# Optimization experiments

Measured on AMD Instinct MI355X. Metric: run time of the kernel, lower is better.

## Reference

```python
import jax, jax.numpy as jnp
import numpy as np

N, E, H, G = 50000, 500000, 64, 64


def _ln(x, g, b):
    m = jnp.mean(x, -1, keepdims=True)
    v = jnp.var(x, -1, keepdims=True)
    return (x - m) * jax.lax.rsqrt(v + 1e-5) * g + b


def _mlp_ln(x, w1, b1, w2, b2, g, be):
    # Linear -> ReLU -> (Dropout eval no-op) -> Linear -> LayerNorm
    h = jax.nn.relu(x @ w1 + b1)
    return _ln(h @ w2 + b2, g, be)


def setup_inputs() -> dict:
    key = jax.random.key(0)
    ks = jax.random.split(key, 24)
    w = lambda i, s: jax.random.normal(ks[i], s, dtype=jnp.float32) * 0.1
    z = lambda s: jnp.zeros(s, jnp.float32)
    o = lambda s: jnp.ones(s, jnp.float32)
    inp = {
        'x': jax.random.normal(ks[0], (N, 3), dtype=jnp.float32),
        'edge_index': jax.random.randint(ks[1], (2, E), 0, N),
        'edge_attr': jax.random.normal(ks[2], (E, 3), dtype=jnp.float32),
        'batch': jnp.sort(jax.random.randint(ks[3], (N,), 0, G)),
        'ne_w1': w(4, (3, H)), 'ne_b1': z((H,)), 'ne_w2': w(5, (H, H)), 'ne_b2': z((H,)), 'ne_g': o((H,)), 'ne_be': z((H,)),
        'ee_w1': w(6, (3, H)), 'ee_b1': z((H,)), 'ee_w2': w(7, (H, H)), 'ee_b2': z((H,)), 'ee_g': o((H,)), 'ee_be': z((H,)),
        'gin0_eps': z((1,)), 'gin0_w1': w(8, (H, H)), 'gin0_b1': z((H,)), 'gin0_w2': w(9, (H, H)), 'gin0_b2': z((H,)), 'gin0_g': o((H,)), 'gin0_be': z((H,)),
        'gin1_eps': z((1,)), 'gin1_w1': w(10, (H, H)), 'gin1_b1': z((H,)), 'gin1_w2': w(11, (H, H)), 'gin1_b2': z((H,)), 'gin1_g': o((H,)), 'gin1_be': z((H,)),
        'gp_w': w(12, (H, H)), 'gp_b': z((H,)), 'gp_g': o((H,)), 'gp_be': z((H,)),
        'ep_w1': w(13, (4 * H, 2 * H)), 'ep_b1': z((2 * H,)),
        'ep_w2': w(14, (2 * H, H)), 'ep_b2': z((H,)),
        'ep_w3': w(15, (H, 1)), 'ep_b3': z((1,)),
    }
    return inp


def reference(x, edge_index, edge_attr, batch,
              ne_w1, ne_b1, ne_w2, ne_b2, ne_g, ne_be,
              ee_w1, ee_b1, ee_w2, ee_b2, ee_g, ee_be,
              gin0_eps, gin0_w1, gin0_b1, gin0_w2, gin0_b2, gin0_g, gin0_be,
              gin1_eps, gin1_w1, gin1_b1, gin1_w2, gin1_b2, gin1_g, gin1_be,
              gp_w, gp_b, gp_g, gp_be,
              ep_w1, ep_b1, ep_w2, ep_b2, ep_w3, ep_b3):
    src, dst = edge_index[0], edge_index[1]
    # encoders
    h = _mlp_ln(x, ne_w1, ne_b1, ne_w2, ne_b2, ne_g, ne_be)            # [N, H]
    ef = _mlp_ln(edge_attr, ee_w1, ee_b1, ee_w2, ee_b2, ee_g, ee_be)   # [E, H]
    # GINEConv layer 0: mlp((1+eps)*x + scatter_add(relu(x_src + e)))
    msg = jax.nn.relu(h[src] + ef)
    aggr = jnp.zeros_like(h).at[dst].add(msg)
    h = _mlp_ln((1.0 + gin0_eps) * h + aggr, gin0_w1, gin0_b1, gin0_w2, gin0_b2, gin0_g, gin0_be)
    h = jax.nn.relu(h)  # inter-layer activation (dropout eval no-op)
    # GINEConv layer 1
    msg = jax.nn.relu(h[src] + ef)
    aggr = jnp.zeros_like(h).at[dst].add(msg)
    h = _mlp_ln((1.0 + gin1_eps) * h + aggr, gin1_w1, gin1_b1, gin1_w2, gin1_b2, gin1_g, gin1_be)
    # global mean pool over graphs
    seg = jax.ops.segment_sum(h, batch, num_segments=G)                            # [G, H]
    cnt = jax.ops.segment_sum(jnp.ones((h.shape[0], 1), h.dtype), batch, num_segments=G)
    gp = seg / jnp.maximum(cnt, 1.0)
    gf = _ln(jax.nn.relu(gp @ gp_w + gp_b), gp_g, gp_be)                           # [G, H]
    # edge predictor on [src | dst | global | edge] = [E, 4H]
    c = jnp.concatenate([h[src], h[dst], gf[batch[src]], ef], axis=-1)
    t = jnp.tanh(c @ ep_w1 + ep_b1)
    t = jnp.tanh(t @ ep_w2 + ep_b2)
    return jax.nn.sigmoid(t @ ep_w3 + ep_b3)  # [E, 1]
```

## Files before the change

### kernel.cpp

```cpp
#include <hip/hip_runtime.h>
#include <hip/hip_bf16.h>

typedef unsigned int uint;
typedef unsigned short ushort;
typedef __attribute__((ext_vector_type(8))) short short8;
typedef __attribute__((ext_vector_type(4))) float floatx4;

__device__ __forceinline__ float bf2f(ushort u) { return __uint_as_float(((uint)u) << 16); }
__device__ __forceinline__ ushort f2bf(float f) {
  uint u = __float_as_uint(f);
  u += 0x7fffu + ((u >> 16) & 1u);
  return (ushort)(u >> 16);
}
__device__ __forceinline__ uint pk2(float a, float b) {
  return (uint)f2bf(a) | ((uint)f2bf(b) << 16);
}
__device__ __forceinline__ float ldf(const void* p, long i, int m) {
  if (m) return bf2f(((const ushort*)p)[i]);
  return ((const float*)p)[i];
}
__device__ __forceinline__ int get_md(const uint* mdp) {
  return (mdp[0] == 0x3F800000u) ? 0 : 1;
}
__device__ __forceinline__ float fast_rcp(float x) { return __builtin_amdgcn_rcpf(x); }
__device__ __forceinline__ float tanh_fast(float x) {
  float e = __builtin_amdgcn_exp2f(2.8853900818f * x);
  return fmaf(-2.f, fast_rcp(1.f + e), 1.f);
}
__device__ __forceinline__ float sigmoid_fast(float x) {
  float e = __builtin_amdgcn_exp2f(-1.4426950409f * x);
  return fast_rcp(1.f + e);
}

__global__ __launch_bounds__(256) void k_enc_mfma(
    const void* __restrict__ in, int R,
    const void* __restrict__ w1, const void* __restrict__ b1,
    const ushort* __restrict__ w2sw_, const void* __restrict__ b2,
    const void* __restrict__ gam, const void* __restrict__ bet,
    ushort* __restrict__ outp, const uint* __restrict__ mdp)
{
  __shared__ float xs[64*3];
  __shared__ float w1s[192], b1s[64], b2s[64], gs[64], bs2[64];
  __shared__ __align__(16) ushort T_s[64 * 72];
  int md = get_md(mdp);
  int tid = threadIdx.x;
  long e0 = (long)blockIdx.x * 64;
  if (tid < 192) {
    w1s[tid] = ldf(w1, tid, md);
    int row = tid / 3, cc = tid - row*3;
    long e = e0 + row;
    xs[tid] = (e < R) ? ldf(in, e*3 + cc, md) : 0.f;
  }
  if (tid < 64) { b1s[tid] = ldf(b1, tid, md); b2s[tid] = ldf(b2, tid, md);
                  gs[tid] = ldf(gam, tid, md); bs2[tid] = ldf(bet, tid, md); }
  __syncthreads();
  int lane = tid & 63, wv = tid >> 6;
  int quad = lane >> 4, mm = lane & 15;
  float x0 = xs[(wv*16 + mm)*3 + 0];
  float x1 = xs[(wv*16 + mm)*3 + 1];
  float x2 = xs[(wv*16 + mm)*3 + 2];
  short8 af[2];
#pragma unroll
  for (int s = 0; s < 2; ++s) {
#pragma unroll
    for (int j = 0; j < 8; ++j) {
      int f = s*32 + quad*8 + j;
      float hv = fmaxf(b1s[f] + x0*w1s[f] + x1*w1s[64+f] + x2*w1s[128+f], 0.f);
      af[s][j] = (short)f2bf(hv);
    }
  }
  floatx4 acc[4] = {};
  const short8* Bp = (const short8*)w2sw_;
#pragma unroll
  for (int s = 0; s < 2; ++s) {
#pragma unroll
    for (int t = 0; t < 4; ++t) {
      short8 b = Bp[(s*4 + t)*64 + lane];
      acc[t] = __builtin_amdgcn_mfma_f32_16x16x32_bf16(af[s], b, acc[t], 0, 0, 0);
    }
  }
  float vv[4][4];
#pragma unroll
  for (int t = 0; t < 4; ++t) {
    float bb = b2s[mm + 16*t];
#pragma unroll
    for (int r = 0; r < 4; ++r) vv[t][r] = acc[t][r] + bb;
  }
  float mr[4], vr[4];
#pragma unroll
  for (int r = 0; r < 4; ++r) {
    float s = vv[0][r] + vv[1][r] + vv[2][r] + vv[3][r];
#pragma unroll
    for (int off = 1; off < 16; off <<= 1) s += __shfl_xor(s, off);
    mr[r] = s * 0.015625f;
    float q = 0.f;
#pragma unroll
    for (int t = 0; t < 4; ++t) { float d = vv[t][r] - mr[r]; q = fmaf(d, d, q); }
#pragma unroll
    for (int off = 1; off < 16; off <<= 1) q += __shfl_xor(q, off);
    vr[r] = rsqrtf(q * 0.015625f + 1e-5f);
  }
#pragma unroll
  for (int t = 0; t < 4; ++t) {
    int col = mm + 16*t;
    float g = gs[col], be = bs2[col];
#pragma unroll
    for (int r = 0; r < 4; ++r)
      T_s[(wv*16 + quad*4 + r)*72 + col] = f2bf((vv[t][r] - mr[r]) * vr[r] * g + be);
  }
  __syncthreads();
#pragma unroll
  for (int i = 0; i < 2; ++i) {
    int gi = tid + 256*i;
    int row = gi >> 3, c = gi & 7;
    long e = e0 + row;
    if (e < R)
      ((uint4*)(outp + e*64))[c] = *(const uint4*)&T_s[row*72 + c*8];
  }
}

__global__ __launch_bounds__(256) void k_deg(
    const int* __restrict__ ei, int* __restrict__ deg, int E_)
{
  int e = blockIdx.x * 256 + threadIdx.x;
  if (e < E_) atomicAdd(&deg[ei[E_ + e]], 1);
}

__global__ __launch_bounds__(256) void k_scan1(
    const int* __restrict__ deg, int* __restrict__ rs, int* __restrict__ bsum, int Nn)
{
  __shared__ int ls[256];
  int tid = threadIdx.x;
  int i = blockIdx.x * 256 + tid;
  int v = (i < Nn) ? deg[i] : 0;
  ls[tid] = v;
  __syncthreads();
  for (int off = 1; off < 256; off <<= 1) {
    int t = (tid >= off) ? ls[tid - off] : 0;
    __syncthreads();
    ls[tid] += t;
    __syncthreads();
  }
  if (i < Nn) rs[i] = ls[tid] - v;
  if (tid == 255) bsum[blockIdx.x] = ls[255];
}

__global__ __launch_bounds__(256) void k_scan2(
    int* __restrict__ bsum, int nb, int* __restrict__ rs, int Nn)
{
  __shared__ int ls[256];
  int tid = threadIdx.x;
  int chunk = (nb + 255) / 256;
  int c0 = tid * chunk, c1 = min(c0 + chunk, nb);
  int sum = 0;
  for (int i = c0; i < c1; ++i) sum += bsum[i];
  ls[tid] = sum;
  __syncthreads();
  for (int off = 1; off < 256; off <<= 1) {
    int t = (tid >= off) ? ls[tid - off] : 0;
    __syncthreads();
    ls[tid] += t;
    __syncthreads();
  }
  int run = ls[tid] - sum;
  for (int i = c0; i < c1; ++i) { int d = bsum[i]; bsum[i] = run; run += d; }
  if (tid == 255) rs[Nn] = ls[255];
}

__global__ __launch_bounds__(256) void k_scan3(
    int* __restrict__ rs, int* __restrict__ cur,
    const int* __restrict__ bsum, int Nn)
{
  int i = blockIdx.x * 256 + threadIdx.x;
  if (i < Nn) {
    int v = rs[i] + bsum[blockIdx.x];
    rs[i] = v;
    cur[i] = v;
  }
}

__global__ __launch_bounds__(256) void k_fill(
    const int* __restrict__ ei, int* __restrict__ cur, int* __restrict__ eidx, int E_)
{
  int e = blockIdx.x * 256 + threadIdx.x;
  if (e < E_) {
    int d = ei[E_ + e];
    int p = atomicAdd(&cur[d], 1);
    eidx[p] = e;
  }
}

__global__ __launch_bounds__(256) void k_aggr(
    const ushort* __restrict__ hbu, const ushort* __restrict__ efu,
    const int* __restrict__ ei, const int* __restrict__ rs,
    const int* __restrict__ eidx, float* __restrict__ aggr, int Nn, int E_)
{
  int gw = (blockIdx.x * 256 + threadIdx.x) >> 6;
  int j = threadIdx.x & 63;
  if (gw >= Nn) return;
  int s0 = rs[gw], s1 = rs[gw + 1];
  float acc = 0.f;
  int idx = s0;
  for (; idx + 2 <= s1; idx += 2) {
    int e1 = eidx[idx], e2 = eidx[idx + 1];
    int sA = ei[e1], sB = ei[e2];
    float hA = bf2f(hbu[(long)sA*64 + j]);
    float fA = bf2f(efu[(long)e1*64 + j]);
    float hB = bf2f(hbu[(long)sB*64 + j]);
    float fB = bf2f(efu[(long)e2*64 + j]);
    acc += fmaxf(hA + fA, 0.f) + fmaxf(hB + fB, 0.f);
  }
  if (idx < s1) {
    int e1 = eidx[idx];
    int sA = ei[e1];
    acc += fmaxf(bf2f(hbu[(long)sA*64 + j]) + bf2f(efu[(long)e1*64 + j]), 0.f);
  }
  aggr[(long)gw*64 + j] = acc;
}

__global__ __launch_bounds__(256) void k_gine_mfma(
    const ushort* __restrict__ hbin, const float* __restrict__ aggr, int Nn,
    const void* __restrict__ epsp,
    const ushort* __restrict__ w1sw_, const void* __restrict__ b1,
    const ushort* __restrict__ w2sw_, const void* __restrict__ b2,
    const void* __restrict__ gam, const void* __restrict__ bet,
    ushort* __restrict__ hbout, int post_relu, const uint* __restrict__ mdp)
{
  __shared__ __align__(16) ushort Ws1[4096], Ws2[4096];
  __shared__ __align__(16) ushort T_s[64 * 72];
  __shared__ float b1s[64], b2s[64], gs[64], bs2[64];
  int md = get_md(mdp);
  int tid = threadIdx.x;
  {
    const uint4* p1 = (const uint4*)w1sw_;
    const uint4* p2 = (const uint4*)w2sw_;
    ((uint4*)Ws1)[tid] = p1[tid];
    ((uint4*)Ws1)[tid + 256] = p1[tid + 256];
    ((uint4*)Ws2)[tid] = p2[tid];
    ((uint4*)Ws2)[tid + 256] = p2[tid + 256];
  }
  if (tid < 64) { b1s[tid] = ldf(b1, tid, md); b2s[tid] = ldf(b2, tid, md);
                  gs[tid] = ldf(gam, tid, md); bs2[tid] = ldf(bet, tid, md); }
  float ope = 1.f + ldf(epsp, 0, md);
  int lane = tid & 63, wv = tid >> 6;
  int quad = lane >> 4, mm = lane & 15;
  long node = (long)blockIdx.x * 64 + wv*16 + mm;
  long nc = (node < Nn) ? node : (long)(Nn - 1);
  const ushort* hrow = hbin + nc*64;
  const float*  arow = aggr + nc*64;
  short8 af[2];
#pragma unroll
  for (int s = 0; s < 2; ++s) {
    int c = s*4 + quad;
    short8 hv = *(const short8*)(hrow + c*8);
    float4 a0 = *(const float4*)(arow + c*8);
    float4 a1 = *(const float4*)(arow + c*8 + 4);
    float uu[8];
    uu[0] = fmaf(bf2f((ushort)hv[0]), ope, a0.x);
    uu[1] = fmaf(bf2f((ushort)hv[1]), ope, a0.y);
    uu[2] = fmaf(bf2f((ushort)hv[2]), ope, a0.z);
    uu[3] = fmaf(bf2f((ushort)hv[3]), ope, a0.w);
    uu[4] = fmaf(bf2f((ushort)hv[4]), ope, a1.x);
    uu[5] = fmaf(bf2f((ushort)hv[5]), ope, a1.y);
    uu[6] = fmaf(bf2f((ushort)hv[6]), ope, a1.z);
    uu[7] = fmaf(bf2f((ushort)hv[7]), ope, a1.w);
#pragma unroll
    for (int j = 0; j < 8; ++j) af[s][j] = (short)f2bf(uu[j]);
  }
  __syncthreads();
  floatx4 acc[4] = {};
#pragma unroll
  for (int s = 0; s < 2; ++s) {
#pragma unroll
    for (int t = 0; t < 4; ++t) {
      short8 b = *(const short8*)&Ws1[((s*4 + t)*64 + lane)*8];
      acc[t] = __builtin_amdgcn_mfma_f32_16x16x32_bf16(af[s], b, acc[t], 0, 0, 0);
    }
  }
#pragma unroll
  for (int t = 0; t < 4; ++t) {
    int col = mm + 16*t;
    float bb = b1s[col];
#pragma unroll
    for (int r = 0; r < 4; ++r)
      T_s[(wv*16 + quad*4 + r)*72 + col] = f2bf(fmaxf(acc[t][r] + bb, 0.f));
  }
  __syncthreads();
  short8 af2[2];
#pragma unroll
  for (int s = 0; s < 2; ++s)
    af2[s] = *(const short8*)&T_s[(wv*16 + mm)*72 + s*32 + quad*8];
  floatx4 acc2[4] = {};
#pragma unroll
  for (int s = 0; s < 2; ++s) {
#pragma unroll
    for (int t = 0; t < 4; ++t) {
      short8 b = *(const short8*)&Ws2[((s*4 + t)*64 + lane)*8];
      acc2[t] = __builtin_amdgcn_mfma_f32_16x16x32_bf16(af2[s], b, acc2[t], 0, 0, 0);
    }
  }
  float vv[4][4];
#pragma unroll
  for (int t = 0; t < 4; ++t) {
    float bb = b2s[mm + 16*t];
#pragma unroll
    for (int r = 0; r < 4; ++r) vv[t][r] = acc2[t][r] + bb;
  }
  float mr[4], vr[4];
#pragma unroll
  for (int r = 0; r < 4; ++r) {
    float s = vv[0][r] + vv[1][r] + vv[2][r] + vv[3][r];
#pragma unroll
    for (int off = 1; off < 16; off <<= 1) s += __shfl_xor(s, off);
    mr[r] = s * 0.015625f;
    float q = 0.f;
#pragma unroll
    for (int t = 0; t < 4; ++t) { float d = vv[t][r] - mr[r]; q = fmaf(d, d, q); }
#pragma unroll
    for (int off = 1; off < 16; off <<= 1) q += __shfl_xor(q, off);
    vr[r] = rsqrtf(q * 0.015625f + 1e-5f);
  }
  __syncthreads();
#pragma unroll
  for (int t = 0; t < 4; ++t) {
    int col = mm + 16*t;
    float g = gs[col], be = bs2[col];
#pragma unroll
    for (int r = 0; r < 4; ++r) {
      float o = (vv[t][r] - mr[r]) * vr[r] * g + be;
      if (post_relu) o = fmaxf(o, 0.f);
      T_s[(wv*16 + quad*4 + r)*72 + col] = f2bf(o);
    }
  }
  __syncthreads();
#pragma unroll
  for (int i = 0; i < 2; ++i) {
    int gi = tid + 256*i;
    int row = gi >> 3, c = gi & 7;
    long n2 = (long)blockIdx.x * 64 + row;
    if (n2 < Nn)
      ((uint4*)(hbout + n2*64))[c] = *(const uint4*)&T_s[row*72 + c*8];
  }
}

__global__ __launch_bounds__(256) void k_pool_f(
    const ushort* __restrict__ hbu, const int* __restrict__ batch,
    float* __restrict__ gsum, float* __restrict__ gcnt, int Nn)
{
  int gw = (blockIdx.x * 256 + threadIdx.x) >> 6;
  int j = threadIdx.x & 63;
  long r0 = (long)gw * 64;
  if (r0 >= Nn) return;
  long rend = min(r0 + 64, (long)Nn);
  float acc = 0.f; int cur = batch[r0]; int run = 0;
  for (long r = r0; r < rend; ++r) {
    int g = batch[r];
    if (g != cur) {
      atomicAdd(&gsum[cur*64 + j], acc);
      if (j == 0) atomicAdd(&gcnt[cur], (float)run);
      acc = 0.f; run = 0; cur = g;
    }
    acc += bf2f(hbu[r*64 + j]);
    run++;
  }
  atomicAdd(&gsum[cur*64 + j], acc);
  if (j == 0) atomicAdd(&gcnt[cur], (float)run);
}

__global__ __launch_bounds__(64) void k_pool_fin_f(
    const float* __restrict__ gsum, const float* __restrict__ gcnt,
    const void* __restrict__ gpw, const void* __restrict__ gpb,
    const void* __restrict__ gpg, const void* __restrict__ gpbe,
    ushort* __restrict__ gfb, const uint* __restrict__ mdp)
{
  __shared__ float wgs[4096];
  __shared__ float us[64];
  int md = get_md(mdp);
  int j = threadIdx.x;
  int g = blockIdx.x;
  for (int i = j; i < 4096; i += 64) wgs[i] = ldf(gpw, i, md);
  float ic = 1.f / fmaxf(gcnt[g], 1.f);
  us[j] = gsum[g*64 + j] * ic;
  __syncthreads();
  float t = ldf(gpb, j, md);
#pragma unroll
  for (int k = 0; k < 64; ++k) t = fmaf(us[k], wgs[k*64 + j], t);
  t = fmaxf(t, 0.f);
  float m = t;
#pragma unroll
  for (int off = 1; off < 64; off <<= 1) m += __shfl_xor(m, off);
  m *= 0.015625f;
  float d = t - m;
  float v = d * d;
#pragma unroll
  for (int off = 1; off < 64; off <<= 1) v += __shfl_xor(v, off);
  float rs = rsqrtf(v * 0.015625f + 1e-5f);
  gfb[g*64 + j] = f2bf(d * rs * ldf(gpg, j, md) + ldf(gpbe, j, md));
}

__global__ __launch_bounds__(256) void k_swz(
    const void* __restrict__ w1, const void* __restrict__ w2,
    const void* __restrict__ w2e, const void* __restrict__ w2n,
    const void* __restrict__ gw10, const void* __restrict__ gw20,
    const void* __restrict__ gw11, const void* __restrict__ gw21,
    ushort* __restrict__ w1sw, ushort* __restrict__ w2sw,
    ushort* __restrict__ ew2sw, ushort* __restrict__ nw2sw,
    ushort* __restrict__ g0w1sw, ushort* __restrict__ g0w2sw,
    ushort* __restrict__ g1w1sw, ushort* __restrict__ g1w2sw,
    const uint* __restrict__ mdp)
{
  int md = get_md(mdp);
  int i = blockIdx.x * 256 + threadIdx.x;
  if (i < 32768) {
    int q = i & 7, lane = (i >> 3) & 63, tt = (i >> 9) & 7, s = i >> 12;
    int k = s*32 + (lane >> 4)*8 + q, n = (lane & 15) + 16*tt;
    w1sw[i] = f2bf(ldf(w1, k*128 + n, md));
  }
  if (i < 8192) {
    int q = i & 7, lane = (i >> 3) & 63, tt = (i >> 9) & 3, s = i >> 11;
    int k = s*32 + (lane >> 4)*8 + q, n = (lane & 15) + 16*tt;
    int src = k*64 + n;
    w2sw[i]   = f2bf(ldf(w2,   src, md));
    ew2sw[i]  = f2bf(ldf(w2e,  src, md));
    nw2sw[i]  = f2bf(ldf(w2n,  src, md));
    g0w1sw[i] = f2bf(ldf(gw10, src, md));
    g0w2sw[i] = f2bf(ldf(gw20, src, md));
    g1w1sw[i] = f2bf(ldf(gw11, src, md));
    g1w2sw[i] = f2bf(ldf(gw21, src, md));
  }
}

__global__ __launch_bounds__(256) void k_pred_mfma(
    const ushort* __restrict__ hb, const ushort* __restrict__ efu,
    const ushort* __restrict__ gfb, const int* __restrict__ ei,
    const int* __restrict__ batch,
    const ushort* __restrict__ w1sw, const ushort* __restrict__ w2sw,
    const void* __restrict__ pb1, const void* __restrict__ pb2,
    const void* __restrict__ pw3, const void* __restrict__ pb3,
    void* __restrict__ out, int E_, const uint* __restrict__ mdp)
{
  __shared__ __align__(16) ushort Ws[8192];
  __shared__ __align__(16) ushort T_s[64 * 136];
  __shared__ float b1s[128], b2s[64], w3s[64];
  int md = get_md(mdp);
  int tid = threadIdx.x;
  if (tid < 128) b1s[tid] = ldf(pb1, tid, md);
  if (tid < 64) { b2s[tid] = ldf(pb2, tid, md); w3s[tid] = ldf(pw3, tid, md); }
  long e0 = (long)blockIdx.x * 64;
  int lane = tid & 63, wv = tid >> 6;
  int quad = lane >> 4, mm = lane & 15;
  long e = e0 + wv*16 + mm;
  if (e >= E_) e = E_ - 1;
  int si = ei[e];
  int di = ei[E_ + e];
  int gi = batch[si];
  const short8* hsrc = (const short8*)(hb  + (long)si*64);
  const short8* hdst = (const short8*)(hb  + (long)di*64);
  const short8* gsrc = (const short8*)(gfb + (long)gi*64);
  const short8* esrc = (const short8*)(efu + e*64);
  short8 af[8];
  af[0] = hsrc[quad]; af[1] = hsrc[4 + quad];
  af[2] = hdst[quad]; af[3] = hdst[4 + quad];
  af[4] = gsrc[quad]; af[5] = gsrc[4 + quad];
  af[6] = esrc[quad]; af[7] = esrc[4 + quad];
  floatx4 acc[8] = {};
  for (int q = 0; q < 4; ++q) {
    __syncthreads();
    const uint4* wp = (const uint4*)(w1sw + q*8192);
#pragma unroll
    for (int i = 0; i < 4; ++i)
      ((uint4*)Ws)[tid + 256*i] = wp[tid + 256*i];
    __syncthreads();
#pragma unroll
    for (int s4 = 0; s4 < 2; ++s4) {
      short8 a = af[q*2 + s4];
#pragma unroll
      for (int t = 0; t < 8; ++t) {
        short8 b = *(const short8*)&Ws[((s4*8 + t)*64 + lane)*8];
        acc[t] = __builtin_amdgcn_mfma_f32_16x16x32_bf16(a, b, acc[t], 0, 0, 0);
      }
    }
  }
#pragma unroll
  for (int t = 0; t < 8; ++t) {
    float bb = b1s[mm + 16*t];
#pragma unroll
    for (int r = 0; r < 4; ++r)
      T_s[(16*wv + quad*4 + r)*136 + mm + 16*t] = f2bf(tanh_fast(acc[t][r] + bb));
  }
  __syncthreads();
  {
    const uint4* wp2 = (const uint4*)w2sw;
#pragma unroll
    for (int i = 0; i < 4; ++i)
      ((uint4*)Ws)[tid + 256*i] = wp2[tid + 256*i];
  }
  __syncthreads();
  floatx4 acc2[4] = {};
#pragma unroll
  for (int s2 = 0; s2 < 4; ++s2) {
    short8 a = *(const short8*)&T_s[(16*wv + mm)*136 + s2*32 + quad*8];
#pragma unroll
    for (int t = 0; t < 4; ++t) {
      short8 b = *(const short8*)&Ws[((s2*4 + t)*64 + lane)*8];
      acc2[t] = __builtin_amdgcn_mfma_f32_16x16x32_bf16(a, b, acc2[t], 0, 0, 0);
    }
  }
  float p0 = 0.f, p1 = 0.f, p2 = 0.f, p3 = 0.f;
#pragma unroll
  for (int t = 0; t < 4; ++t) {
    int col = mm + 16*t;
    float bb = b2s[col], w3v = w3s[col];
    p0 = fmaf(tanh_fast(acc2[t][0] + bb), w3v, p0);
    p1 = fmaf(tanh_fast(acc2[t][1] + bb), w3v, p1);
    p2 = fmaf(tanh_fast(acc2[t][2] + bb), w3v, p2);
    p3 = fmaf(tanh_fast(acc2[t][3] + bb), w3v, p3);
  }
#pragma unroll
  for (int off = 1; off < 16; off <<= 1) {
    p0 += __shfl_xor(p0, off);
    p1 += __shfl_xor(p1, off);
    p2 += __shfl_xor(p2, off);
    p3 += __shfl_xor(p3, off);
  }
  if (mm == 0) {
    float b3 = ldf(pb3, 0, md);
    long eb = e0 + 16*wv + quad*4;
    float ps[4] = {p0, p1, p2, p3};
#pragma unroll
    for (int r = 0; r < 4; ++r) {
      if (eb + r < E_) {
        float sg = sigmoid_fast(ps[r] + b3);
        if (md) ((ushort*)out)[eb + r] = f2bf(sg);
        else    ((float*)out)[eb + r]  = sg;
      }
    }
  }
}

extern "C" void kernel_launch(void* const* d_in, const int* in_sizes, int n_in,
                              void* d_out, int out_size, void* d_ws, size_t ws_size,
                              hipStream_t stream)
{
  const void* x     = d_in[0];
  const int*  ei    = (const int*)d_in[1];
  const void* eattr = d_in[2];
  const int*  batch = (const int*)d_in[3];
  const void* ne_w1 = d_in[4];  const void* ne_b1 = d_in[5];
  const void* ne_w2 = d_in[6];  const void* ne_b2 = d_in[7];
  const void* ne_g  = d_in[8];  const void* ne_be = d_in[9];
  const void* ee_w1 = d_in[10]; const void* ee_b1 = d_in[11];
  const void* ee_w2 = d_in[12]; const void* ee_b2 = d_in[13];
  const void* ee_g  = d_in[14]; const void* ee_be = d_in[15];
  const void* g0_ep = d_in[16];
  const void* g0_w1 = d_in[17]; const void* g0_b1 = d_in[18];
  const void* g0_w2 = d_in[19]; const void* g0_b2 = d_in[20];
  const void* g0_g  = d_in[21]; const void* g0_be = d_in[22];
  const void* g1_ep = d_in[23];
  const void* g1_w1 = d_in[24]; const void* g1_b1 = d_in[25];
  const void* g1_w2 = d_in[26]; const void* g1_b2 = d_in[27];
  const void* g1_g  = d_in[28]; const void* g1_be = d_in[29];
  const void* gp_w  = d_in[30]; const void* gp_b  = d_in[31];
  const void* gp_g  = d_in[32]; const void* gp_be = d_in[33];
  const void* ep_w1 = d_in[34]; const void* ep_b1 = d_in[35];
  const void* ep_w2 = d_in[36]; const void* ep_b2 = d_in[37];
  const void* ep_w3 = d_in[38]; const void* ep_b3 = d_in[39];

  int N = in_sizes[3];
  int E = in_sizes[1] / 2;
  const uint* mdp = (const uint*)ne_g;

  char* ws = (char*)d_ws;
  size_t off = 0;
  auto alloc = [&](size_t bytes) { char* p = ws + off; off += (bytes + 255) & ~(size_t)255; return p; };
  ushort* hb     = (ushort*)alloc((size_t)N * 64 * 2);
  ushort* efu    = (ushort*)alloc((size_t)E * 64 * 2);
  float*  aggr   = (float*) alloc((size_t)N * 64 * 4);
  float*  gsum   = (float*) alloc(64 * 64 * 4);
  float*  gcnt   = (float*) alloc(64 * 4);
  ushort* gfb    = (ushort*)alloc(64 * 64 * 2);
  ushort* w1sw   = (ushort*)alloc(32768 * 2);
  ushort* w2sw   = (ushort*)alloc(8192 * 2);
  ushort* ew2sw  = (ushort*)alloc(8192 * 2);
  ushort* nw2sw  = (ushort*)alloc(8192 * 2);
  ushort* g0w1sw = (ushort*)alloc(8192 * 2);
  ushort* g0w2sw = (ushort*)alloc(8192 * 2);
  ushort* g1w1sw = (ushort*)alloc(8192 * 2);
  ushort* g1w2sw = (ushort*)alloc(8192 * 2);
  int*    deg    = (int*)   alloc((size_t)N * 4);
  int*    rs     = (int*)   alloc((size_t)(N + 1) * 4);
  int*    cur    = (int*)   alloc((size_t)N * 4);
  int*    eidx   = (int*)   alloc((size_t)E * 4);
  int*    bsum   = (int*)   alloc((size_t)((N + 255) / 256) * 4);
  (void)ws_size; (void)n_in; (void)out_size;

  int gN = (N + 255) / 256;
  int gE = (E + 255) / 256;
  int gE64 = (E + 63) / 64;
  int gN64 = (N + 63) / 64;
  int gAggr = (int)(((long)N * 64 + 255) / 256);
  int gPool = ((N + 63) / 64 + 3) / 4;

  hipMemsetAsync(deg, 0, (size_t)N * 4, stream);
  hipMemsetAsync(gsum, 0, 64 * 64 * 4 + 256, stream);

  k_swz<<<128, 256, 0, stream>>>(ep_w1, ep_w2, ee_w2, ne_w2, g0_w1, g0_w2, g1_w1, g1_w2,
                                 w1sw, w2sw, ew2sw, nw2sw,
                                 g0w1sw, g0w2sw, g1w1sw, g1w2sw, mdp);
  k_deg<<<gE, 256, 0, stream>>>(ei, deg, E);
  k_scan1<<<gN, 256, 0, stream>>>(deg, rs, bsum, N);
  k_scan2<<<1, 256, 0, stream>>>(bsum, gN, rs, N);
  k_scan3<<<gN, 256, 0, stream>>>(rs, cur, bsum, N);
  k_fill<<<gE, 256, 0, stream>>>(ei, cur, eidx, E);
  k_enc_mfma<<<gN64, 256, 0, stream>>>(x, N, ne_w1, ne_b1, nw2sw, ne_b2, ne_g, ne_be, hb, mdp);
  k_enc_mfma<<<gE64, 256, 0, stream>>>(eattr, E, ee_w1, ee_b1, ew2sw, ee_b2, ee_g, ee_be, efu, mdp);
  k_aggr<<<gAggr, 256, 0, stream>>>(hb, efu, ei, rs, eidx, aggr, N, E);
  k_gine_mfma<<<gN64, 256, 0, stream>>>(hb, aggr, N, g0_ep, g0w1sw, g0_b1, g0w2sw, g0_b2,
                                        g0_g, g0_be, hb, 1, mdp);
  k_aggr<<<gAggr, 256, 0, stream>>>(hb, efu, ei, rs, eidx, aggr, N, E);
  k_gine_mfma<<<gN64, 256, 0, stream>>>(hb, aggr, N, g1_ep, g1w1sw, g1_b1, g1w2sw, g1_b2,
                                        g1_g, g1_be, hb, 0, mdp);
  k_pool_f<<<gPool, 256, 0, stream>>>(hb, batch, gsum, gcnt, N);
  k_pool_fin_f<<<64, 64, 0, stream>>>(gsum, gcnt, gp_w, gp_b, gp_g, gp_be, gfb, mdp);
  k_pred_mfma<<<gE64, 256, 0, stream>>>(hb, efu, gfb, ei, batch, w1sw, w2sw,
                                        ep_b1, ep_b2, ep_w3, ep_b3, d_out, E, mdp);
}
```

Measured before the change: 475.6 us.

## Store (edge,src) pairs in CSR and process 128 edges per predictor block

The CSR fill now stores the source node next to each edge id as an int2, so the aggregation kernel skips a dependent gather through edge_index. The edge predictor block now handles two 64-edge tiles at once, so each staged weight chunk in shared memory feeds twice as many MFMAs and the per-block weight reloads are halved. In exchange the predictor uses more registers and shared memory per block, which may lower occupancy, and the CSR array doubles in size.

```diff
diff --git a/kernel.cpp b/kernel.cpp
--- a/kernel.cpp
+++ b/kernel.cpp
@@ -180,20 +180,22 @@
 }
 
 __global__ __launch_bounds__(256) void k_fill(
-    const int* __restrict__ ei, int* __restrict__ cur, int* __restrict__ eidx, int E_)
+    const int* __restrict__ ei, int* __restrict__ cur,
+    int2* __restrict__ ep, int E_)
 {
   int e = blockIdx.x * 256 + threadIdx.x;
   if (e < E_) {
+    int s = ei[e];
     int d = ei[E_ + e];
     int p = atomicAdd(&cur[d], 1);
-    eidx[p] = e;
+    ep[p] = make_int2(e, s);
   }
 }
 
 __global__ __launch_bounds__(256) void k_aggr(
     const ushort* __restrict__ hbu, const ushort* __restrict__ efu,
-    const int* __restrict__ ei, const int* __restrict__ rs,
-    const int* __restrict__ eidx, float* __restrict__ aggr, int Nn, int E_)
+    const int2* __restrict__ ep, const int* __restrict__ rs,
+    float* __restrict__ aggr, int Nn)
 {
   int gw = (blockIdx.x * 256 + threadIdx.x) >> 6;
   int j = threadIdx.x & 63;
@@ -202,18 +204,17 @@
   float acc = 0.f;
   int idx = s0;
   for (; idx + 2 <= s1; idx += 2) {
-    int e1 = eidx[idx], e2 = eidx[idx + 1];
-    int sA = ei[e1], sB = ei[e2];
-    float hA = bf2f(hbu[(long)sA*64 + j]);
-    float fA = bf2f(efu[(long)e1*64 + j]);
-    float hB = bf2f(hbu[(long)sB*64 + j]);
-    float fB = bf2f(efu[(long)e2*64 + j]);
+    int2 a = ep[idx];
+    int2 b = ep[idx + 1];
+    float hA = bf2f(hbu[(long)a.y*64 + j]);
+    float fA = bf2f(efu[(long)a.x*64 + j]);
+    float hB = bf2f(hbu[(long)b.y*64 + j]);
+    float fB = bf2f(efu[(long)b.x*64 + j]);
     acc += fmaxf(hA + fA, 0.f) + fmaxf(hB + fB, 0.f);
   }
   if (idx < s1) {
-    int e1 = eidx[idx];
-    int sA = ei[e1];
-    acc += fmaxf(bf2f(hbu[(long)sA*64 + j]) + bf2f(efu[(long)e1*64 + j]), 0.f);
+    int2 a = ep[idx];
+    acc += fmaxf(bf2f(hbu[(long)a.y*64 + j]) + bf2f(efu[(long)a.x*64 + j]), 0.f);
   }
   aggr[(long)gw*64 + j] = acc;
 }
@@ -440,31 +441,29 @@
     void* __restrict__ out, int E_, const uint* __restrict__ mdp)
 {
   __shared__ __align__(16) ushort Ws[8192];
-  __shared__ __align__(16) ushort T_s[64 * 136];
+  __shared__ __align__(16) ushort T_s[128 * 136];
   __shared__ float b1s[128], b2s[64], w3s[64];
   int md = get_md(mdp);
   int tid = threadIdx.x;
   if (tid < 128) b1s[tid] = ldf(pb1, tid, md);
   if (tid < 64) { b2s[tid] = ldf(pb2, tid, md); w3s[tid] = ldf(pw3, tid, md); }
-  long e0 = (long)blockIdx.x * 64;
+  long e0 = (long)blockIdx.x * 128;
   int lane = tid & 63, wv = tid >> 6;
   int quad = lane >> 4, mm = lane & 15;
-  long e = e0 + wv*16 + mm;
-  if (e >= E_) e = E_ - 1;
-  int si = ei[e];
-  int di = ei[E_ + e];
-  int gi = batch[si];
-  const short8* hsrc = (const short8*)(hb  + (long)si*64);
-  const short8* hdst = (const short8*)(hb  + (long)di*64);
-  const short8* gsrc = (const short8*)(gfb + (long)gi*64);
-  const short8* esrc = (const short8*)(efu + e*64);
-  short8 af[8];
-  af[0] = hsrc[quad]; af[1] = hsrc[4 + quad];
-  af[2] = hdst[quad]; af[3] = hdst[4 + quad];
-  af[4] = gsrc[quad]; af[5] = gsrc[4 + quad];
-  af[6] = esrc[quad]; af[7] = esrc[4 + quad];
-  floatx4 acc[8] = {};
+  long eA = e0 + wv*16 + mm;      if (eA >= E_) eA = E_ - 1;
+  long eB = e0 + 64 + wv*16 + mm; if (eB >= E_) eB = E_ - 1;
+  int siA = ei[eA], diA = ei[E_ + eA], giA = batch[siA];
+  int siB = ei[eB], diB = ei[E_ + eB], giB = batch[siB];
+  const short8* srcA[4] = {
+    (const short8*)(hb  + (long)siA*64), (const short8*)(hb  + (long)diA*64),
+    (const short8*)(gfb + (long)giA*64), (const short8*)(efu + eA*64) };
+  const short8* srcB[4] = {
+    (const short8*)(hb  + (long)siB*64), (const short8*)(hb  + (long)diB*64),
+    (const short8*)(gfb + (long)giB*64), (const short8*)(efu + eB*64) };
+  floatx4 accA[8] = {}, accB[8] = {};
   for (int q = 0; q < 4; ++q) {
+    short8 a0A = srcA[q][quad], a1A = srcA[q][4 + quad];
+    short8 a0B = srcB[q][quad], a1B = srcB[q][4 + quad];
     __syncthreads();
     const uint4* wp = (const uint4*)(w1sw + q*8192);
 #pragma unroll
@@ -472,21 +471,23 @@
       ((uint4*)Ws)[tid + 256*i] = wp[tid + 256*i];
     __syncthreads();
 #pragma unroll
-    for (int s4 = 0; s4 < 2; ++s4) {
-      short8 a = af[q*2 + s4];
-#pragma unroll
-      for (int t = 0; t < 8; ++t) {
-        short8 b = *(const short8*)&Ws[((s4*8 + t)*64 + lane)*8];
-        acc[t] = __builtin_amdgcn_mfma_f32_16x16x32_bf16(a, b, acc[t], 0, 0, 0);
-      }
+    for (int t = 0; t < 8; ++t) {
+      short8 b0 = *(const short8*)&Ws[((0*8 + t)*64 + lane)*8];
+      accA[t] = __builtin_amdgcn_mfma_f32_16x16x32_bf16(a0A, b0, accA[t], 0, 0, 0);
+      accB[t] = __builtin_amdgcn_mfma_f32_16x16x32_bf16(a0B, b0, accB[t], 0, 0, 0);
+      short8 b1 = *(const short8*)&Ws[((1*8 + t)*64 + lane)*8];
+      accA[t] = __builtin_amdgcn_mfma_f32_16x16x32_bf16(a1A, b1, accA[t], 0, 0, 0);
+      accB[t] = __builtin_amdgcn_mfma_f32_16x16x32_bf16(a1B, b1, accB[t], 0, 0, 0);
     }
   }
 #pragma unroll
   for (int t = 0; t < 8; ++t) {
     float bb = b1s[mm + 16*t];
 #pragma unroll
-    for (int r = 0; r < 4; ++r)
-      T_s[(16*wv + quad*4 + r)*136 + mm + 16*t] = f2bf(tanh_fast(acc[t][r] + bb));
+    for (int r = 0; r < 4; ++r) {
+      T_s[(16*wv + quad*4 + r)*136 + mm + 16*t]        = f2bf(tanh_fast(accA[t][r] + bb));
+      T_s[(64 + 16*wv + quad*4 + r)*136 + mm + 16*t]   = f2bf(tanh_fast(accB[t][r] + bb));
+    }
   }
   __syncthreads();
   {
@@ -496,43 +497,57 @@
       ((uint4*)Ws)[tid + 256*i] = wp2[tid + 256*i];
   }
   __syncthreads();
-  floatx4 acc2[4] = {};
+  floatx4 acc2A[4] = {}, acc2B[4] = {};
 #pragma unroll
   for (int s2 = 0; s2 < 4; ++s2) {
-    short8 a = *(const short8*)&T_s[(16*wv + mm)*136 + s2*32 + quad*8];
+    short8 aA = *(const short8*)&T_s[(16*wv + mm)*136 + s2*32 + quad*8];
+    short8 aB = *(const short8*)&T_s[(64 + 16*wv + mm)*136 + s2*32 + quad*8];
 #pragma unroll
     for (int t = 0; t < 4; ++t) {
       short8 b = *(const short8*)&Ws[((s2*4 + t)*64 + lane)*8];
-      acc2[t] = __builtin_amdgcn_mfma_f32_16x16x32_bf16(a, b, acc2[t], 0, 0, 0);
-    }
-  }
-  float p0 = 0.f, p1 = 0.f, p2 = 0.f, p3 = 0.f;
+      acc2A[t] = __builtin_amdgcn_mfma_f32_16x16x32_bf16(aA, b, acc2A[t], 0, 0, 0);
+      acc2B[t] = __builtin_amdgcn_mfma_f32_16x16x32_bf16(aB, b, acc2B[t], 0, 0, 0);
+    }
+  }
+  float pA0 = 0.f, pA1 = 0.f, pA2 = 0.f, pA3 = 0.f;
+  float pB0 = 0.f, pB1 = 0.f, pB2 = 0.f, pB3 = 0.f;
 #pragma unroll
   for (int t = 0; t < 4; ++t) {
     int col = mm + 16*t;
     float bb = b2s[col], w3v = w3s[col];
-    p0 = fmaf(tanh_fast(acc2[t][0] + bb), w3v, p0);
-    p1 = fmaf(tanh_fast(acc2[t][1] + bb), w3v, p1);
-    p2 = fmaf(tanh_fast(acc2[t][2] + bb), w3v, p2);
-    p3 = fmaf(tanh_fast(acc2[t][3] + bb), w3v, p3);
+    pA0 = fmaf(tanh_fast(acc2A[t][0] + bb), w3v, pA0);
+    pA1 = fmaf(tanh_fast(acc2A[t][1] + bb), w3v, pA1);
+    pA2 = fmaf(tanh_fast(acc2A[t][2] + bb), w3v, pA2);
+    pA3 = fmaf(tanh_fast(acc2A[t][3] + bb), w3v, pA3);
+    pB0 = fmaf(tanh_fast(acc2B[t][0] + bb), w3v, pB0);
+    pB1 = fmaf(tanh_fast(acc2B[t][1] + bb), w3v, pB1);
+    pB2 = fmaf(tanh_fast(acc2B[t][2] + bb), w3v, pB2);
+    pB3 = fmaf(tanh_fast(acc2B[t][3] + bb), w3v, pB3);
   }
 #pragma unroll
   for (int off = 1; off < 16; off <<= 1) {
-    p0 += __shfl_xor(p0, off);
-    p1 += __shfl_xor(p1, off);
-    p2 += __shfl_xor(p2, off);
-    p3 += __shfl_xor(p3, off);
+    pA0 += __shfl_xor(pA0, off); pA1 += __shfl_xor(pA1, off);
+    pA2 += __shfl_xor(pA2, off); pA3 += __shfl_xor(pA3, off);
+    pB0 += __shfl_xor(pB0, off); pB1 += __shfl_xor(pB1, off);
+    pB2 += __shfl_xor(pB2, off); pB3 += __shfl_xor(pB3, off);
   }
   if (mm == 0) {
     float b3 = ldf(pb3, 0, md);
-    long eb = e0 + 16*wv + quad*4;
-    float ps[4] = {p0, p1, p2, p3};
+    float psA[4] = {pA0, pA1, pA2, pA3};
+    float psB[4] = {pB0, pB1, pB2, pB3};
+    long ebA = e0 + 16*wv + quad*4;
+    long ebB = e0 + 64 + 16*wv + quad*4;
 #pragma unroll
     for (int r = 0; r < 4; ++r) {
-      if (eb + r < E_) {
-        float sg = sigmoid_fast(ps[r] + b3);
-        if (md) ((ushort*)out)[eb + r] = f2bf(sg);
-        else    ((float*)out)[eb + r]  = sg;
+      if (ebA + r < E_) {
+        float sg = sigmoid_fast(psA[r] + b3);
+        if (md) ((ushort*)out)[ebA + r] = f2bf(sg);
+        else    ((float*)out)[ebA + r]  = sg;
+      }
+      if (ebB + r < E_) {
+        float sg = sigmoid_fast(psB[r] + b3);
+        if (md) ((ushort*)out)[ebB + r] = f2bf(sg);
+        else    ((float*)out)[ebB + r]  = sg;
       }
     }
   }
@@ -590,13 +605,14 @@
   int*    deg    = (int*)   alloc((size_t)N * 4);
   int*    rs     = (int*)   alloc((size_t)(N + 1) * 4);
   int*    cur    = (int*)   alloc((size_t)N * 4);
-  int*    eidx   = (int*)   alloc((size_t)E * 4);
+  int2*   ep     = (int2*)  alloc((size_t)E * 8);
   int*    bsum   = (int*)   alloc((size_t)((N + 255) / 256) * 4);
   (void)ws_size; (void)n_in; (void)out_size;
 
   int gN = (N + 255) / 256;
   int gE = (E + 255) / 256;
   int gE64 = (E + 63) / 64;
+  int gE128 = (E + 127) / 128;
   int gN64 = (N + 63) / 64;
   int gAggr = (int)(((long)N * 64 + 255) / 256);
   int gPool = ((N + 63) / 64 + 3) / 4;
@@ -611,17 +627,17 @@
   k_scan1<<<gN, 256, 0, stream>>>(deg, rs, bsum, N);
   k_scan2<<<1, 256, 0, stream>>>(bsum, gN, rs, N);
   k_scan3<<<gN, 256, 0, stream>>>(rs, cur, bsum, N);
-  k_fill<<<gE, 256, 0, stream>>>(ei, cur, eidx, E);
+  k_fill<<<gE, 256, 0, stream>>>(ei, cur, ep, E);
   k_enc_mfma<<<gN64, 256, 0, stream>>>(x, N, ne_w1, ne_b1, nw2sw, ne_b2, ne_g, ne_be, hb, mdp);
   k_enc_mfma<<<gE64, 256, 0, stream>>>(eattr, E, ee_w1, ee_b1, ew2sw, ee_b2, ee_g, ee_be, efu, mdp);
-  k_aggr<<<gAggr, 256, 0, stream>>>(hb, efu, ei, rs, eidx, aggr, N, E);
+  k_aggr<<<gAggr, 256, 0, stream>>>(hb, efu, ep, rs, aggr, N);
   k_gine_mfma<<<gN64, 256, 0, stream>>>(hb, aggr, N, g0_ep, g0w1sw, g0_b1, g0w2sw, g0_b2,
                                         g0_g, g0_be, hb, 1, mdp);
-  k_aggr<<<gAggr, 256, 0, stream>>>(hb, efu, ei, rs, eidx, aggr, N, E);
+  k_aggr<<<gAggr, 256, 0, stream>>>(hb, efu, ep, rs, aggr, N);
   k_gine_mfma<<<gN64, 256, 0, stream>>>(hb, aggr, N, g1_ep, g1w1sw, g1_b1, g1w2sw, g1_b2,
                                         g1_g, g1_be, hb, 0, mdp);
   k_pool_f<<<gPool, 256, 0, stream>>>(hb, batch, gsum, gcnt, N);
   k_pool_fin_f<<<64, 64, 0, stream>>>(gsum, gcnt, gp_w, gp_b, gp_g, gp_be, gfb, mdp);
-  k_pred_mfma<<<gE64, 256, 0, stream>>>(hb, efu, gfb, ei, batch, w1sw, w2sw,
-                                        ep_b1, ep_b2, ep_w3, ep_b3, d_out, E, mdp);
-}
+  k_pred_mfma<<<gE128, 256, 0, stream>>>(hb, efu, gfb, ei, batch, w1sw, w2sw,
+                                         ep_b1, ep_b2, ep_w3, ep_b3, d_out, E, mdp);
+}
```

After: 466.8 us. Within noise of the previous version (-1.9%).

## Make edge predictor persistent with resident LDS weights; store src in CSR entries

Applied to the files above, without the earlier changes.

The edge predictor becomes a persistent kernel with 512-thread blocks. Each block loads both predictor weight matrices into LDS once, then loops over 128-edge tiles, prefetching the next tile's gathered features into registers. This removes the repeated per-block weight staging and barriers, at the cost of large LDS use and low occupancy. The CSR fill now stores (edge, src) pairs, so aggregation skips a dependent index lookup.

```diff
diff --git a/kernel.cpp b/kernel.cpp
--- a/kernel.cpp
+++ b/kernel.cpp
@@ -180,20 +180,22 @@
 }
 
 __global__ __launch_bounds__(256) void k_fill(
-    const int* __restrict__ ei, int* __restrict__ cur, int* __restrict__ eidx, int E_)
+    const int* __restrict__ ei, int* __restrict__ cur,
+    int2* __restrict__ ep, int E_)
 {
   int e = blockIdx.x * 256 + threadIdx.x;
   if (e < E_) {
+    int s = ei[e];
     int d = ei[E_ + e];
     int p = atomicAdd(&cur[d], 1);
-    eidx[p] = e;
+    ep[p] = make_int2(e, s);
   }
 }
 
 __global__ __launch_bounds__(256) void k_aggr(
     const ushort* __restrict__ hbu, const ushort* __restrict__ efu,
-    const int* __restrict__ ei, const int* __restrict__ rs,
-    const int* __restrict__ eidx, float* __restrict__ aggr, int Nn, int E_)
+    const int2* __restrict__ ep, const int* __restrict__ rs,
+    float* __restrict__ aggr, int Nn)
 {
   int gw = (blockIdx.x * 256 + threadIdx.x) >> 6;
   int j = threadIdx.x & 63;
@@ -202,18 +204,17 @@
   float acc = 0.f;
   int idx = s0;
   for (; idx + 2 <= s1; idx += 2) {
-    int e1 = eidx[idx], e2 = eidx[idx + 1];
-    int sA = ei[e1], sB = ei[e2];
-    float hA = bf2f(hbu[(long)sA*64 + j]);
-    float fA = bf2f(efu[(long)e1*64 + j]);
-    float hB = bf2f(hbu[(long)sB*64 + j]);
-    float fB = bf2f(efu[(long)e2*64 + j]);
+    int2 a = ep[idx];
+    int2 b = ep[idx + 1];
+    float hA = bf2f(hbu[(long)a.y*64 + j]);
+    float fA = bf2f(efu[(long)a.x*64 + j]);
+    float hB = bf2f(hbu[(long)b.y*64 + j]);
+    float fB = bf2f(efu[(long)b.x*64 + j]);
     acc += fmaxf(hA + fA, 0.f) + fmaxf(hB + fB, 0.f);
   }
   if (idx < s1) {
-    int e1 = eidx[idx];
-    int sA = ei[e1];
-    acc += fmaxf(bf2f(hbu[(long)sA*64 + j]) + bf2f(efu[(long)e1*64 + j]), 0.f);
+    int2 a = ep[idx];
+    acc += fmaxf(bf2f(hbu[(long)a.y*64 + j]) + bf2f(efu[(long)a.x*64 + j]), 0.f);
   }
   aggr[(long)gw*64 + j] = acc;
 }
@@ -430,7 +431,7 @@
   }
 }
 
-__global__ __launch_bounds__(256) void k_pred_mfma(
+__global__ __launch_bounds__(512) void k_pred_persist(
     const ushort* __restrict__ hb, const ushort* __restrict__ efu,
     const ushort* __restrict__ gfb, const int* __restrict__ ei,
     const int* __restrict__ batch,
@@ -439,100 +440,105 @@
     const void* __restrict__ pw3, const void* __restrict__ pb3,
     void* __restrict__ out, int E_, const uint* __restrict__ mdp)
 {
-  __shared__ __align__(16) ushort Ws[8192];
-  __shared__ __align__(16) ushort T_s[64 * 136];
+  __shared__ __align__(16) ushort W1s[32768];
+  __shared__ __align__(16) ushort W2s[8192];
+  __shared__ __align__(16) ushort T_s[128 * 136];
   __shared__ float b1s[128], b2s[64], w3s[64];
   int md = get_md(mdp);
   int tid = threadIdx.x;
+  for (int i = tid; i < 4096; i += 512) ((uint4*)W1s)[i] = ((const uint4*)w1sw)[i];
+  for (int i = tid; i < 1024; i += 512) ((uint4*)W2s)[i] = ((const uint4*)w2sw)[i];
   if (tid < 128) b1s[tid] = ldf(pb1, tid, md);
   if (tid < 64) { b2s[tid] = ldf(pb2, tid, md); w3s[tid] = ldf(pw3, tid, md); }
-  long e0 = (long)blockIdx.x * 64;
+  float b3 = ldf(pb3, 0, md);
+  __syncthreads();
   int lane = tid & 63, wv = tid >> 6;
   int quad = lane >> 4, mm = lane & 15;
-  long e = e0 + wv*16 + mm;
-  if (e >= E_) e = E_ - 1;
-  int si = ei[e];
-  int di = ei[E_ + e];
-  int gi = batch[si];
-  const short8* hsrc = (const short8*)(hb  + (long)si*64);
-  const short8* hdst = (const short8*)(hb  + (long)di*64);
-  const short8* gsrc = (const short8*)(gfb + (long)gi*64);
-  const short8* esrc = (const short8*)(efu + e*64);
-  short8 af[8];
-  af[0] = hsrc[quad]; af[1] = hsrc[4 + quad];
-  af[2] = hdst[quad]; af[3] = hdst[4 + quad];
-  af[4] = gsrc[quad]; af[5] = gsrc[4 + quad];
-  af[6] = esrc[quad]; af[7] = esrc[4 + quad];
-  floatx4 acc[8] = {};
-  for (int q = 0; q < 4; ++q) {
-    __syncthreads();
-    const uint4* wp = (const uint4*)(w1sw + q*8192);
-#pragma unroll
-    for (int i = 0; i < 4; ++i)
-      ((uint4*)Ws)[tid + 256*i] = wp[tid + 256*i];
-    __syncthreads();
-#pragma unroll
-    for (int s4 = 0; s4 < 2; ++s4) {
-      short8 a = af[q*2 + s4];
+  long nTiles = (E_ + 127) >> 7;
+  short8 afN[8];
+  long tile = blockIdx.x;
+  if (tile < nTiles) {
+    long e = tile*128 + wv*16 + mm; if (e >= E_) e = E_ - 1;
+    int si = ei[e], di = ei[E_ + e], gi = batch[si];
+    const short8* hs = (const short8*)(hb  + (long)si*64);
+    const short8* hd = (const short8*)(hb  + (long)di*64);
+    const short8* gs = (const short8*)(gfb + (long)gi*64);
+    const short8* es = (const short8*)(efu + e*64);
+    afN[0]=hs[quad]; afN[1]=hs[4+quad];
+    afN[2]=hd[quad]; afN[3]=hd[4+quad];
+    afN[4]=gs[quad]; afN[5]=gs[4+quad];
+    afN[6]=es[quad]; afN[7]=es[4+quad];
+  }
+  for (; tile < nTiles; tile += gridDim.x) {
+    short8 af[8];
+#pragma unroll
+    for (int i = 0; i < 8; ++i) af[i] = afN[i];
+    long nt = tile + gridDim.x;
+    if (nt < nTiles) {
+      long e = nt*128 + wv*16 + mm; if (e >= E_) e = E_ - 1;
+      int si = ei[e], di = ei[E_ + e], gi = batch[si];
+      const short8* hs = (const short8*)(hb  + (long)si*64);
+      const short8* hd = (const short8*)(hb  + (long)di*64);
+      const short8* gs = (const short8*)(gfb + (long)gi*64);
+      const short8* es = (const short8*)(efu + e*64);
+      afN[0]=hs[quad]; afN[1]=hs[4+quad];
+      afN[2]=hd[quad]; afN[3]=hd[4+quad];
+      afN[4]=gs[quad]; afN[5]=gs[4+quad];
+      afN[6]=es[quad]; afN[7]=es[4+quad];
+    }
+    floatx4 acc[8] = {};
+#pragma unroll
+    for (int s = 0; s < 8; ++s) {
 #pragma unroll
       for (int t = 0; t < 8; ++t) {
-        short8 b = *(const short8*)&Ws[((s4*8 + t)*64 + lane)*8];
-        acc[t] = __builtin_amdgcn_mfma_f32_16x16x32_bf16(a, b, acc[t], 0, 0, 0);
+        short8 b = *(const short8*)&W1s[((s*8 + t)*64 + lane)*8];
+        acc[t] = __builtin_amdgcn_mfma_f32_16x16x32_bf16(af[s], b, acc[t], 0, 0, 0);
       }
     }
-  }
-#pragma unroll
-  for (int t = 0; t < 8; ++t) {
-    float bb = b1s[mm + 16*t];
-#pragma unroll
-    for (int r = 0; r < 4; ++r)
-      T_s[(16*wv + quad*4 + r)*136 + mm + 16*t] = f2bf(tanh_fast(acc[t][r] + bb));
-  }
-  __syncthreads();
-  {
-    const uint4* wp2 = (const uint4*)w2sw;
-#pragma unroll
-    for (int i = 0; i < 4; ++i)
-      ((uint4*)Ws)[tid + 256*i] = wp2[tid + 256*i];
-  }
-  __syncthreads();
-  floatx4 acc2[4] = {};
-#pragma unroll
-  for (int s2 = 0; s2 < 4; ++s2) {
-    short8 a = *(const short8*)&T_s[(16*wv + mm)*136 + s2*32 + quad*8];
+#pragma unroll
+    for (int t = 0; t < 8; ++t) {
+      float bb = b1s[mm + 16*t];
+#pragma unroll
+      for (int r = 0; r < 4; ++r)
+        T_s[(16*wv + quad*4 + r)*136 + mm + 16*t] = f2bf(tanh_fast(acc[t][r] + bb));
+    }
+    floatx4 acc2[4] = {};
+#pragma unroll
+    for (int s2 = 0; s2 < 4; ++s2) {
+      short8 a = *(const short8*)&T_s[(16*wv + mm)*136 + s2*32 + quad*8];
+#pragma unroll
+      for (int t = 0; t < 4; ++t) {
+        short8 b = *(const short8*)&W2s[((s2*4 + t)*64 + lane)*8];
+        acc2[t] = __builtin_amdgcn_mfma_f32_16x16x32_bf16(a, b, acc2[t], 0, 0, 0);
+      }
+    }
+    float p0 = 0.f, p1 = 0.f, p2 = 0.f, p3 = 0.f;
 #pragma unroll
     for (int t = 0; t < 4; ++t) {
-      short8 b = *(const short8*)&Ws[((s2*4 + t)*64 + lane)*8];
-      acc2[t] = __builtin_amdgcn_mfma_f32_16x16x32_bf16(a, b, acc2[t], 0, 0, 0);
-    }
-  }
-  float p0 = 0.f, p1 = 0.f, p2 = 0.f, p3 = 0.f;
-#pragma unroll
-  for (int t = 0; t < 4; ++t) {
-    int col = mm + 16*t;
-    float bb = b2s[col], w3v = w3s[col];
-    p0 = fmaf(tanh_fast(acc2[t][0] + bb), w3v, p0);
-    p1 = fmaf(tanh_fast(acc2[t][1] + bb), w3v, p1);
-    p2 = fmaf(tanh_fast(acc2[t][2] + bb), w3v, p2);
-    p3 = fmaf(tanh_fast(acc2[t][3] + bb), w3v, p3);
-  }
-#pragma unroll
-  for (int off = 1; off < 16; off <<= 1) {
-    p0 += __shfl_xor(p0, off);
-    p1 += __shfl_xor(p1, off);
-    p2 += __shfl_xor(p2, off);
-    p3 += __shfl_xor(p3, off);
-  }
-  if (mm == 0) {
-    float b3 = ldf(pb3, 0, md);
-    long eb = e0 + 16*wv + quad*4;
-    float ps[4] = {p0, p1, p2, p3};
-#pragma unroll
-    for (int r = 0; r < 4; ++r) {
-      if (eb + r < E_) {
-        float sg = sigmoid_fast(ps[r] + b3);
-        if (md) ((ushort*)out)[eb + r] = f2bf(sg);
-        else    ((float*)out)[eb + r]  = sg;
+      int col = mm + 16*t;
+      float bb = b2s[col], w3v = w3s[col];
+      p0 = fmaf(tanh_fast(acc2[t][0] + bb), w3v, p0);
+      p1 = fmaf(tanh_fast(acc2[t][1] + bb), w3v, p1);
+      p2 = fmaf(tanh_fast(acc2[t][2] + bb), w3v, p2);
+      p3 = fmaf(tanh_fast(acc2[t][3] + bb), w3v, p3);
+    }
+#pragma unroll
+    for (int off = 1; off < 16; off <<= 1) {
+      p0 += __shfl_xor(p0, off);
+      p1 += __shfl_xor(p1, off);
+      p2 += __shfl_xor(p2, off);
+      p3 += __shfl_xor(p3, off);
+    }
+    if (mm == 0) {
+      long eb = tile*128 + 16*wv + quad*4;
+      float ps[4] = {p0, p1, p2, p3};
+#pragma unroll
+      for (int r = 0; r < 4; ++r) {
+        if (eb + r < E_) {
+          float sg = sigmoid_fast(ps[r] + b3);
+          if (md) ((ushort*)out)[eb + r] = f2bf(sg);
+          else    ((float*)out)[eb + r]  = sg;
+        }
       }
     }
   }
@@ -590,7 +596,7 @@
   int*    deg    = (int*)   alloc((size_t)N * 4);
   int*    rs     = (int*)   alloc((size_t)(N + 1) * 4);
   int*    cur    = (int*)   alloc((size_t)N * 4);
-  int*    eidx   = (int*)   alloc((size_t)E * 4);
+  int2*   ep     = (int2*)  alloc((size_t)E * 8);
   int*    bsum   = (int*)   alloc((size_t)((N + 255) / 256) * 4);
   (void)ws_size; (void)n_in; (void)out_size;
 
@@ -611,17 +617,17 @@
   k_scan1<<<gN, 256, 0, stream>>>(deg, rs, bsum, N);
   k_scan2<<<1, 256, 0, stream>>>(bsum, gN, rs, N);
   k_scan3<<<gN, 256, 0, stream>>>(rs, cur, bsum, N);
-  k_fill<<<gE, 256, 0, stream>>>(ei, cur, eidx, E);
+  k_fill<<<gE, 256, 0, stream>>>(ei, cur, ep, E);
   k_enc_mfma<<<gN64, 256, 0, stream>>>(x, N, ne_w1, ne_b1, nw2sw, ne_b2, ne_g, ne_be, hb, mdp);
   k_enc_mfma<<<gE64, 256, 0, stream>>>(eattr, E, ee_w1, ee_b1, ew2sw, ee_b2, ee_g, ee_be, efu, mdp);
-  k_aggr<<<gAggr, 256, 0, stream>>>(hb, efu, ei, rs, eidx, aggr, N, E);
+  k_aggr<<<gAggr, 256, 0, stream>>>(hb, efu, ep, rs, aggr, N);
   k_gine_mfma<<<gN64, 256, 0, stream>>>(hb, aggr, N, g0_ep, g0w1sw, g0_b1, g0w2sw, g0_b2,
                                         g0_g, g0_be, hb, 1, mdp);
-  k_aggr<<<gAggr, 256, 0, stream>>>(hb, efu, ei, rs, eidx, aggr, N, E);
+  k_aggr<<<gAggr, 256, 0, stream>>>(hb, efu, ep, rs, aggr, N);
   k_gine_mfma<<<gN64, 256, 0, stream>>>(hb, aggr, N, g1_ep, g1w1sw, g1_b1, g1w2sw, g1_b2,
                                         g1_g, g1_be, hb, 0, mdp);
   k_pool_f<<<gPool, 256, 0, stream>>>(hb, batch, gsum, gcnt, N);
   k_pool_fin_f<<<64, 64, 0, stream>>>(gsum, gcnt, gp_w, gp_b, gp_g, gp_be, gfb, mdp);
-  k_pred_mfma<<<gE64, 256, 0, stream>>>(hb, efu, gfb, ei, batch, w1sw, w2sw,
-                                        ep_b1, ep_b2, ep_w3, ep_b3, d_out, E, mdp);
-}
+  k_pred_persist<<<256, 512, 0, stream>>>(hb, efu, gfb, ei, batch, w1sw, w2sw,
+                                          ep_b1, ep_b2, ep_w3, ep_b3, d_out, E, mdp);
+}
```

Result: no change. 466.3 us (-2.0%).
